# Optimization experiments

Measured on AMD Instinct MI355X. Metric: run time of the kernel, lower is better.

Reference implementation:

```python
import jax, jax.numpy as jnp
import numpy as np
import math

EMB = 512
HID = 512
SEQ = 128
BATCH = 64
VOCAB = 10000
NUM_LAYERS = 2


def setup_inputs() -> dict:
    key = jax.random.key(0)
    ks = jax.random.split(key, 16)
    inputs = jax.random.randint(ks[0], (SEQ, BATCH), 0, VOCAB)
    hidden = jnp.zeros((NUM_LAYERS, BATCH, HID), dtype=jnp.float32)
    emb_table = jax.random.normal(ks[1], (VOCAB, EMB), dtype=jnp.float32) * 0.02

    def lin(k, fan_in, fan_out):
        bound = 1.0 / math.sqrt(fan_in)
        kw, kb = jax.random.split(k)
        W = jax.random.uniform(kw, (fan_in, fan_out), minval=-bound, maxval=bound, dtype=jnp.float32)
        b = jax.random.uniform(kb, (fan_out,), minval=-bound, maxval=bound, dtype=jnp.float32)
        return W, b

    # layer 0: input_size = emb + hid; layer 1: input_size = 2*hid
    Wg0, bg0 = lin(ks[2], EMB + HID, 2 * HID)
    Wc0, bc0 = lin(ks[3], EMB + HID, HID)
    Wg1, bg1 = lin(ks[4], 2 * HID, 2 * HID)
    Wc1, bc1 = lin(ks[5], 2 * HID, HID)
    Wout, bout = lin(ks[6], HID, VOCAB)
    return {
        "inputs": inputs, "hidden": hidden, "emb_table": emb_table,
        "Wg0": Wg0, "bg0": bg0, "Wc0": Wc0, "bc0": bc0,
        "Wg1": Wg1, "bg1": bg1, "Wc1": Wc1, "bc1": bc1,
        "Wout": Wout, "bout": bout,
    }


def _gru_forward(inputs, hidden, emb_table, layer_params, Wout, bout):
    # embeddings: [S, B, E], scaled like WordEmbedding
    emb = emb_table[inputs] * jnp.asarray(math.sqrt(EMB), emb_table.dtype)

    def step(h, x_t):
        layer_in = x_t
        new_h = []
        for n, (Wg, bg, Wc, bc) in enumerate(layer_params):
            g = jax.nn.sigmoid(jnp.concatenate([layer_in, h[n]], axis=1) @ Wg + bg)
            update = g[:, :HID]
            reset = g[:, HID:]
            cell = jnp.tanh(jnp.concatenate([layer_in, reset * h[n]], axis=1) @ Wc + bc)
            h_out = (1.0 - update) * h[n] + update * cell
            new_h.append(h_out)
            layer_in = h_out
        logits_t = layer_in @ Wout + bout  # [B, V]
        return jnp.stack(new_h, axis=0), logits_t

    hidden_final, logits = jax.lax.scan(step, hidden, emb)
    return logits, hidden_final  # [S, B, V], [L, B, H]


def reference(inputs, hidden, emb_table, Wg0, bg0, Wc0, bc0, Wg1, bg1, Wc1, bc1, Wout, bout):
    layer_params = [(Wg0, bg0, Wc0, bc0), (Wg1, bg1, Wc1, bc1)]
    return _gru_forward(inputs, hidden, emb_table, layer_params, Wout, bout)
```

## Files before the change

### kernel.cpp

```cpp
#include <hip/hip_runtime.h>
#include <cstdint>
#include <cstddef>

#define SEQ 128
#define BATCH 64
#define NVOCAB 10000
#define NREC 64
#define NWORK 192
#define NTOT 256

typedef __attribute__((ext_vector_type(8))) short short8;
typedef __attribute__((ext_vector_type(4))) float f32x4;

__device__ __forceinline__ unsigned short f2b(float f) {
  union { float f; unsigned u; } c; c.f = f;
  unsigned u = c.u;
  unsigned r = (u + 0x7fffu + ((u >> 16) & 1u)) >> 16;
  return (unsigned short)r;
}

__device__ __forceinline__ f32x4 mfma16(short8 a, short8 b, f32x4 c) {
  return __builtin_amdgcn_mfma_f32_16x16x32_bf16(a, b, c, 0, 0, 0);
}

__device__ __forceinline__ short8 ldg_coh(const unsigned short* p) {
  short8 r;
  asm volatile("global_load_dwordx4 %0, %1, off sc0 sc1" : "=v"(r) : "v"(p));
  return r;
}
__device__ __forceinline__ void stg_coh(unsigned short* p, short8 v) {
  asm volatile("global_store_dwordx4 %0, %1, off sc0 sc1" :: "v"(p), "v"(v) : "memory");
}
__device__ __forceinline__ void st_stamp(int* p, int v) {
  asm volatile("global_store_dword %0, %1, off sc0 sc1" :: "v"(p), "v"(v) : "memory");
}
__device__ __forceinline__ int ld_stamp(const int* p) {
  int r;
  asm volatile("global_load_dword %0, %1, off sc0 sc1" : "=v"(r) : "v"(p));
  return r;
}

template<int SLP>
__device__ __forceinline__ void wait_all32(const int* rep, int need) {
  if (need < 0) return;
  int idx = threadIdx.x & 31;
  int guard = 0;
  for (;;) {
    int v = ld_stamp(rep + idx);
    asm volatile("s_waitcnt vmcnt(0)" ::: "memory");
    if (__all(v >= need)) return;
    __builtin_amdgcn_s_sleep(SLP);
    if (++guard > 3000000) return;
  }
}

__global__ void pack_frag(const float* __restrict__ src, unsigned short* __restrict__ dst,
                          int ksteps, int row_off, int src_ld, int ntiles, int mode, int nreal) {
  int tid = blockIdx.x * 256 + threadIdx.x;
  int total = ntiles * ksteps * 64;
  if (tid >= total) return;
  int l = tid & 63;
  int ks = (tid >> 6) % ksteps;
  int nt = tid / (64 * ksteps);
  int n = nt * 16 + (l & 15);
  int col;
  bool valid = true;
  if (mode == 1) {
    int jc = n >> 5, s = n & 31;
    col = (s < 16) ? (16 * jc + s) : (512 + 16 * jc + (s - 16));
  } else {
    col = n;
    valid = (n < nreal);
  }
  int k0 = row_off + ks * 32 + ((l >> 4) << 3);
  short8 o;
  for (int j = 0; j < 8; ++j) {
    float x = valid ? src[(size_t)(k0 + j) * src_ld + col] : 0.f;
    o[j] = (short)f2b(x);
  }
  *reinterpret_cast<short8*>(&dst[(size_t)tid * 8]) = o;
}

__global__ void pack_bias(const float* __restrict__ bg0, const float* __restrict__ bg1,
                          float* __restrict__ bg0p, float* __restrict__ bg1p) {
  int p = blockIdx.x * 256 + threadIdx.x;
  if (p >= 1024) return;
  int jc = p >> 5, s = p & 31;
  int col = (s < 16) ? (16 * jc + s) : (512 + 16 * jc + (s - 16));
  bg0p[p] = bg0[col];
  bg1p[p] = bg1[col];
}

__global__ void embed_gather(const int* __restrict__ inp, const float* __restrict__ tab,
                             unsigned short* __restrict__ XA) {
  int tid = blockIdx.x * 256 + threadIdx.x;
  if (tid >= SEQ * 64 * 64) return;
  int row = tid & 63;
  int kt = (tid >> 6) & 63;
  int t = tid >> 12;
  int v = inp[t * BATCH + row];
  const float* s = &tab[(size_t)v * 512 + kt * 8];
  const float scale = 22.627416997969522f;
  short8 o;
  for (int j = 0; j < 8; ++j) o[j] = (short)f2b(s[j] * scale);
  *reinterpret_cast<short8*>(&XA[(size_t)tid * 8]) = o;
}

__global__ void init_states(const float* __restrict__ hid, unsigned short* __restrict__ H0INITB,
                            unsigned short* __restrict__ H1INITB, int* __restrict__ stamps) {
  int idx = blockIdx.x * 256 + threadIdx.x;
  if (idx < 24 * 64) stamps[idx] = -1;
  if (idx >= 64 * 512) return;
  int row = idx >> 9, c = idx & 511;
  size_t ko = (((size_t)(c >> 3)) * 64 + row) * 8 + (c & 7);
  H0INITB[ko] = f2b(hid[idx]);
  H1INITB[ko] = f2b(hid[64 * 512 + idx]);
}

__launch_bounds__(256, 2)
__global__ void gemm128(const unsigned short* __restrict__ A, const unsigned short* __restrict__ Bf,
                        const float* __restrict__ bias, float* __restrict__ C,
                        int Nld, int Nreal) {
  __shared__ __align__(16) unsigned short ldsA[16 * 512];
  __shared__ __align__(16) unsigned short ldsB[16 * 512];
  int nb = blockIdx.x, yb = blockIdx.y;
  int l = threadIdx.x & 63, w = threadIdx.x >> 6;
  int mh = w >> 1, nh = w & 1;
  f32x4 acc[4][4] = {};
  for (int ko = 0; ko < 8; ++ko) {
    __syncthreads();
    for (int j = 0; j < 4; ++j) {
      int c = w * 4 + j;
      int m8 = c >> 1, ks = c & 1;
      int t = yb * 2 + (m8 >> 2);
      int kt = ko * 8 + ks * 4 + (l >> 4);
      int row = (m8 & 3) * 16 + (l & 15);
      size_t gidx = (((size_t)t * 64 + kt) * 64 + row) * 8;
      *reinterpret_cast<short8*>(&ldsA[(size_t)c * 512 + l * 8]) =
          *reinterpret_cast<const short8*>(&A[gidx]);
      size_t gb = (((size_t)(nb * 8 + (c >> 1)) * 16) + (size_t)(ko * 2 + (c & 1))) * 512 + (size_t)l * 8;
      *reinterpret_cast<short8*>(&ldsB[(size_t)c * 512 + l * 8]) =
          *reinterpret_cast<const short8*>(&Bf[gb]);
    }
    __syncthreads();
    for (int ks = 0; ks < 2; ++ks) {
      short8 a[4], b[4];
      for (int mt = 0; mt < 4; ++mt) {
        int m8 = mh * 4 + mt;
        a[mt] = *reinterpret_cast<const short8*>(&ldsA[((size_t)(m8 * 2 + ks) * 64 + l) * 8]);
      }
      for (int nt = 0; nt < 4; ++nt) {
        int n8 = nh * 4 + nt;
        b[nt] = *reinterpret_cast<const short8*>(&ldsB[((size_t)(n8 * 2 + ks) * 64 + l) * 8]);
      }
      for (int mt = 0; mt < 4; ++mt)
        for (int nt = 0; nt < 4; ++nt)
          acc[mt][nt] = mfma16(a[mt], b[nt], acc[mt][nt]);
    }
  }
  for (int mt = 0; mt < 4; ++mt) {
    for (int nt = 0; nt < 4; ++nt) {
      int col = nb * 128 + nh * 64 + nt * 16 + (l & 15);
      if (col >= Nreal) continue;
      float bv = bias[col];
      int row0 = yb * 128 + mh * 64 + mt * 16 + ((l >> 4) << 2);
      for (int r = 0; r < 4; ++r)
        C[(size_t)(row0 + r) * Nld + col] = acc[mt][nt][r] + bv;
    }
  }
}

template<int KS, int LAYER>
__device__ void rec_layer(
    int g, const unsigned short* __restrict__ Wg, const unsigned short* __restrict__ Wc,
    const float* __restrict__ Xg0p, const float* __restrict__ Xc0p,
    const float* __restrict__ bg1p, const float* __restrict__ bc1,
    const float* __restrict__ hidden,
    unsigned short* __restrict__ H0ALL, unsigned short* __restrict__ H1ALL,
    const unsigned short* __restrict__ H0INITB, const unsigned short* __restrict__ H1INITB,
    unsigned short* __restrict__ RH0, unsigned short* __restrict__ RH1,
    int* __restrict__ stamps, float* __restrict__ hidden_out,
    float (&red)[4][64][33], float (&u_lds)[64][17], float (&hf)[64][17]) {
  constexpr int KQ = KS / 4;
  const int tid = threadIdx.x;
  const int l = tid & 63, w = tid >> 6;
  const int s = l & 15, q = l >> 4;

  int* SR   = stamps + (LAYER ? 4 : 0) * 64;
  int* SH0  = stamps + 8 * 64;
  int* SH1  = stamps + 12 * 64;
  int* SHW  = stamps + 16 * 64;
  int* mySH = LAYER ? SH1 : SH0;
  const int repw = ((g + w) & 3) * 64;
  unsigned short* myRH = LAYER ? RH1 : RH0;

  short8 bg[2][KQ];
  short8 bc[KQ];
#pragma unroll
  for (int kk = 0; kk < KQ; ++kk) {
    int ks = w * KQ + kk;
    bg[0][kk] = *reinterpret_cast<const short8*>(&Wg[(((size_t)(2 * g) * KS + ks) * 64 + l) * 8]);
    bg[1][kk] = *reinterpret_cast<const short8*>(&Wg[(((size_t)(2 * g + 1) * KS + ks) * 64 + l) * 8]);
    bc[kk]    = *reinterpret_cast<const short8*>(&Wc[(((size_t)g * KS + ks) * 64 + l) * 8]);
  }

  {
    int col = tid & 15;
#pragma unroll
    for (int rr = 0; rr < 4; ++rr) {
      int row = (tid >> 4) * 4 + rr;
      hf[row][col] = hidden[(size_t)LAYER * 32768 + (size_t)row * 512 + 16 * g + col];
    }
  }
  __syncthreads();

  for (int t = 0; t < 128; ++t) {
    float xg[8], xc[8];
    if constexpr (LAYER == 0) {
      int row = tid & 63;
      int kg = (tid >> 6) & 1;
      int base = (tid < 128) ? 16 : 0;
#pragma unroll
      for (int j = 0; j < 8; ++j)
        xg[j] = Xg0p[((size_t)(t * 64 + row)) * 1024 + g * 32 + base + kg * 8 + j];
#pragma unroll
      for (int j = 0; j < 8; ++j)
        xc[j] = Xc0p[((size_t)(t * 64 + row)) * 512 + 16 * g + kg * 8 + j];
    }

    const unsigned short* A0 = LAYER ? (H0ALL + (size_t)t * 32768)
                                     : (t ? (H0ALL + (size_t)(t - 1) * 32768) : H0INITB);
    const unsigned short* A1 = nullptr;
    if (LAYER) A1 = t ? (H1ALL + (size_t)(t - 1) * 32768) : H1INITB;

    {
      f32x4 acc[4][2] = {};
      if constexpr (LAYER == 0) {
        wait_all32<1>(SH0 + repw, t - 1);
        short8 a[4][4];
#pragma unroll
        for (int kk2 = 0; kk2 < 4; ++kk2) {
          int kl = w * 4 + kk2;
#pragma unroll
          for (int mt = 0; mt < 4; ++mt)
            a[kk2][mt] = ldg_coh(&A0[(((size_t)(kl * 4 + q)) * 64 + mt * 16 + s) * 8]);
        }
        asm volatile("s_waitcnt vmcnt(0)" ::: "memory");
        __builtin_amdgcn_sched_barrier(0);
#pragma unroll
        for (int kk2 = 0; kk2 < 4; ++kk2)
#pragma unroll
          for (int mt = 0; mt < 4; ++mt) {
            acc[mt][0] = mfma16(a[kk2][mt], bg[0][kk2], acc[mt][0]);
            acc[mt][1] = mfma16(a[kk2][mt], bg[1][kk2], acc[mt][1]);
          }
      } else {
        if (w >= 2) wait_all32<1>(SH1 + repw, t - 1);
        else        wait_all32<1>(SH0 + repw, t);
        const unsigned short* ab = (w >= 2) ? A1 : A0;
#pragma unroll
        for (int hb = 0; hb < 2; ++hb) {
          short8 a[4][4];
#pragma unroll
          for (int kk2 = 0; kk2 < 4; ++kk2) {
            int kl = ((w & 1) * 8 + hb * 4 + kk2);
#pragma unroll
            for (int mt = 0; mt < 4; ++mt)
              a[kk2][mt] = ldg_coh(&ab[(((size_t)(kl * 4 + q)) * 64 + mt * 16 + s) * 8]);
          }
          asm volatile("s_waitcnt vmcnt(0)" ::: "memory");
          __builtin_amdgcn_sched_barrier(0);
#pragma unroll
          for (int kk2 = 0; kk2 < 4; ++kk2)
#pragma unroll
            for (int mt = 0; mt < 4; ++mt) {
              acc[mt][0] = mfma16(a[kk2][mt], bg[0][hb * 4 + kk2], acc[mt][0]);
              acc[mt][1] = mfma16(a[kk2][mt], bg[1][hb * 4 + kk2], acc[mt][1]);
            }
        }
      }
#pragma unroll
      for (int mt = 0; mt < 4; ++mt)
#pragma unroll
        for (int nt = 0; nt < 2; ++nt)
#pragma unroll
          for (int r = 0; r < 4; ++r)
            red[w][mt * 16 + q * 4 + r][nt * 16 + s] = acc[mt][nt][r];
    }
    __syncthreads();
    if (tid < 128) {
      int row = tid & 63, kg = tid >> 6;
      short8 o;
#pragma unroll
      for (int j = 0; j < 8; ++j) {
        int col = 16 + kg * 8 + j;
        float sum = red[0][row][col] + red[1][row][col] + red[2][row][col] + red[3][row][col];
        sum += LAYER ? bg1p[g * 32 + col] : xg[j];
        float gate = 1.f / (1.f + __expf(-sum));
        o[j] = (short)f2b(gate * hf[row][kg * 8 + j]);
      }
      stg_coh(&myRH[((size_t)(2 * g + kg) * 64 + row) * 8], o);
    } else {
      int t2 = tid - 128;
      int row = t2 & 63, kg = t2 >> 6;
#pragma unroll
      for (int j = 0; j < 8; ++j) {
        int col = kg * 8 + j;
        float sum = red[0][row][col] + red[1][row][col] + red[2][row][col] + red[3][row][col];
        sum += LAYER ? bg1p[g * 32 + col] : xg[j];
        u_lds[row][col] = 1.f / (1.f + __expf(-sum));
      }
    }
    asm volatile("s_waitcnt vmcnt(0)" ::: "memory");
    __syncthreads();
    if (tid == 0) {
#pragma unroll
      for (int r = 0; r < 4; ++r) st_stamp(&SR[r * 64 + g], t);
    }

    {
      f32x4 acc[4] = {};
      if constexpr (LAYER == 0) {
        wait_all32<1>(SR + repw, t);
        short8 a[4][4];
#pragma unroll
        for (int kk2 = 0; kk2 < 4; ++kk2) {
          int kl = w * 4 + kk2;
#pragma unroll
          for (int mt = 0; mt < 4; ++mt)
            a[kk2][mt] = ldg_coh(&myRH[(((size_t)(kl * 4 + q)) * 64 + mt * 16 + s) * 8]);
        }
        asm volatile("s_waitcnt vmcnt(0)" ::: "memory");
        __builtin_amdgcn_sched_barrier(0);
#pragma unroll
        for (int kk2 = 0; kk2 < 4; ++kk2)
#pragma unroll
          for (int mt = 0; mt < 4; ++mt)
            acc[mt] = mfma16(a[kk2][mt], bc[kk2], acc[mt]);
      } else {
        if (w >= 2) wait_all32<1>(SR + repw, t);
        const unsigned short* ab = (w >= 2) ? myRH : A0;
#pragma unroll
        for (int hb = 0; hb < 2; ++hb) {
          short8 a[4][4];
#pragma unroll
          for (int kk2 = 0; kk2 < 4; ++kk2) {
            int kl = ((w & 1) * 8 + hb * 4 + kk2);
#pragma unroll
            for (int mt = 0; mt < 4; ++mt)
              a[kk2][mt] = ldg_coh(&ab[(((size_t)(kl * 4 + q)) * 64 + mt * 16 + s) * 8]);
          }
          asm volatile("s_waitcnt vmcnt(0)" ::: "memory");
          __builtin_amdgcn_sched_barrier(0);
#pragma unroll
          for (int kk2 = 0; kk2 < 4; ++kk2)
#pragma unroll
            for (int mt = 0; mt < 4; ++mt)
              acc[mt] = mfma16(a[kk2][mt], bc[hb * 4 + kk2], acc[mt]);
        }
      }
#pragma unroll
      for (int mt = 0; mt < 4; ++mt)
#pragma unroll
        for (int r = 0; r < 4; ++r)
          red[w][mt * 16 + q * 4 + r][s] = acc[mt][r];
    }
    __syncthreads();
    if (tid < 128) {
      int row = tid & 63, kg = tid >> 6;
      short8 o;
#pragma unroll
      for (int j = 0; j < 8; ++j) {
        int cl = kg * 8 + j;
        float sum = red[0][row][cl] + red[1][row][cl] + red[2][row][cl] + red[3][row][cl];
        sum += LAYER ? bc1[16 * g + cl] : xc[j];
        float cv = tanhf(sum);
        float u = u_lds[row][cl];
        float hp = hf[row][cl];
        float hn = hp + u * (cv - hp);
        hf[row][cl] = hn;
        o[j] = (short)f2b(hn);
      }
      size_t ko = ((size_t)(2 * g + kg) * 64 + row) * 8;
      if (LAYER == 0) stg_coh(&H0ALL[(size_t)t * 32768 + ko], o);
      else            stg_coh(&H1ALL[(size_t)t * 32768 + ko], o);
    }
    asm volatile("s_waitcnt vmcnt(0)" ::: "memory");
    __syncthreads();
    if (tid == 0) {
#pragma unroll
      for (int r = 0; r < 4; ++r) st_stamp(&mySH[r * 64 + g], t);
      if (LAYER) {
#pragma unroll
        for (int r = 0; r < 8; ++r) st_stamp(&SHW[r * 64 + g], t);
      }
    }
  }

  {
    int col = tid & 15;
#pragma unroll
    for (int rr = 0; rr < 4; ++rr) {
      int row = (tid >> 4) * 4 + rr;
      hidden_out[(size_t)LAYER * 32768 + (size_t)row * 512 + 16 * g + col] = hf[row][col];
    }
  }
}

__device__ void worker_path(int wid, const unsigned short* __restrict__ A,
                            const unsigned short* __restrict__ Bf,
                            const float* __restrict__ bias, float* __restrict__ C,
                            const int* __restrict__ stamps, char* smem) {
  unsigned short* ldsA = (unsigned short*)smem;
  unsigned short* ldsB = (unsigned short*)(smem + 16384);
  const int* rep = stamps + (16 + (wid & 7)) * 64;
  int l = threadIdx.x & 63, w = threadIdx.x >> 6;
  int mh = w >> 1, nh = w & 1;
  for (int id = wid; id < 64 * 80; id += NWORK) {
    int tp = id / 80, nb = id - tp * 80;
    wait_all32<16>(rep, 2 * tp + 1);
    f32x4 acc[4][4] = {};
    for (int ko = 0; ko < 8; ++ko) {
      __syncthreads();
      for (int j = 0; j < 4; ++j) {
        int c = w * 4 + j;
        int m8 = c >> 1, ks = c & 1;
        int t = tp * 2 + (m8 >> 2);
        int kt = ko * 8 + ks * 4 + (l >> 4);
        int row = (m8 & 3) * 16 + (l & 15);
        size_t gidx = (((size_t)t * 64 + kt) * 64 + row) * 8;
        *reinterpret_cast<short8*>(&ldsA[(size_t)c * 512 + l * 8]) =
            *reinterpret_cast<const short8*>(&A[gidx]);
        size_t gb = (((size_t)(nb * 8 + (c >> 1)) * 16) + (size_t)(ko * 2 + (c & 1))) * 512 + (size_t)l * 8;
        *reinterpret_cast<short8*>(&ldsB[(size_t)c * 512 + l * 8]) =
            *reinterpret_cast<const short8*>(&Bf[gb]);
      }
      __syncthreads();
      for (int ks = 0; ks < 2; ++ks) {
        short8 a[4], b[4];
        for (int mt = 0; mt < 4; ++mt)
          a[mt] = *reinterpret_cast<const short8*>(&ldsA[((size_t)((mh * 4 + mt) * 2 + ks) * 64 + l) * 8]);
        for (int nt = 0; nt < 4; ++nt)
          b[nt] = *reinterpret_cast<const short8*>(&ldsB[((size_t)((nh * 4 + nt) * 2 + ks) * 64 + l) * 8]);
        for (int mt = 0; mt < 4; ++mt)
          for (int nt = 0; nt < 4; ++nt)
            acc[mt][nt] = mfma16(a[mt], b[nt], acc[mt][nt]);
      }
    }
    for (int mt = 0; mt < 4; ++mt) {
      for (int nt = 0; nt < 4; ++nt) {
        int col = nb * 128 + nh * 64 + nt * 16 + (l & 15);
        if (col >= NVOCAB) continue;
        float bv = bias[col];
        int row0 = tp * 128 + mh * 64 + mt * 16 + ((l >> 4) << 2);
        for (int r = 0; r < 4; ++r)
          C[(size_t)(row0 + r) * NVOCAB + col] = acc[mt][nt][r] + bv;
      }
    }
  }
}

__launch_bounds__(256, 1)
__global__ void fused_persist(const unsigned short* __restrict__ Wg0h, const unsigned short* __restrict__ Wc0h,
                              const unsigned short* __restrict__ Wg1, const unsigned short* __restrict__ Wc1,
                              const float* __restrict__ Xg0p, const float* __restrict__ Xc0p,
                              const float* __restrict__ bg1p, const float* __restrict__ bc1,
                              const float* __restrict__ hidden,
                              unsigned short* __restrict__ H0ALL, unsigned short* __restrict__ H1ALL,
                              const unsigned short* __restrict__ H0INITB, const unsigned short* __restrict__ H1INITB,
                              unsigned short* __restrict__ RH0, unsigned short* __restrict__ RH1,
                              int* __restrict__ stamps, float* __restrict__ hidden_out,
                              const unsigned short* __restrict__ Wout_f, const float* __restrict__ bout,
                              float* __restrict__ out) {
  __shared__ __align__(16) char smem[42496];
  int wg = blockIdx.x;
  if (wg >= NREC) {
    worker_path(wg - NREC, H1ALL, Wout_f, bout, out, stamps, smem);
    return;
  }
  float (*red)[64][33] = (float(*)[64][33])smem;
  float (*u_lds)[17] = (float(*)[17])(smem + 33792);
  float (*hf)[17] = (float(*)[17])(smem + 38144);
  int g = wg & 31;
  if (wg < 32)
    rec_layer<16, 0>(g, Wg0h, Wc0h, Xg0p, Xc0p, bg1p, bc1, hidden, H0ALL, H1ALL,
                     H0INITB, H1INITB, RH0, RH1, stamps, hidden_out,
                     *(float(*)[4][64][33])red, *(float(*)[64][17])u_lds, *(float(*)[64][17])hf);
  else
    rec_layer<32, 1>(g, Wg1, Wc1, Xg0p, Xc0p, bg1p, bc1, hidden, H0ALL, H1ALL,
                     H0INITB, H1INITB, RH0, RH1, stamps, hidden_out,
                     *(float(*)[4][64][33])red, *(float(*)[64][17])u_lds, *(float(*)[64][17])hf);
}

static inline int gridFor(long long n) { return (int)((n + 255) / 256); }

extern "C" void kernel_launch(void* const* d_in, const int* in_sizes, int n_in,
                              void* d_out, int out_size, void* d_ws, size_t ws_size,
                              hipStream_t stream) {
  const int*   inputs = (const int*)d_in[0];
  const float* hidden = (const float*)d_in[1];
  const float* embtab = (const float*)d_in[2];
  const float* Wg0 = (const float*)d_in[3];
  const float* bg0 = (const float*)d_in[4];
  const float* Wc0 = (const float*)d_in[5];
  const float* bc0 = (const float*)d_in[6];
  const float* Wg1 = (const float*)d_in[7];
  const float* bg1 = (const float*)d_in[8];
  const float* Wc1 = (const float*)d_in[9];
  const float* bc1 = (const float*)d_in[10];
  const float* Wout = (const float*)d_in[11];
  const float* bout = (const float*)d_in[12];
  float* out = (float*)d_out;

  char* p = (char*)d_ws;
  size_t off = 0;
  auto carve = [&](size_t bytes) { char* r = p + off; off += (bytes + 255) & ~(size_t)255; return (void*)r; };
  unsigned short* XA     = (unsigned short*)carve((size_t)8192 * 512 * 2);
  unsigned short* Wg0x_f = (unsigned short*)carve((size_t)512 * 1024 * 2);
  unsigned short* Wg0h_f = (unsigned short*)carve((size_t)512 * 1024 * 2);
  unsigned short* Wc0x_f = (unsigned short*)carve((size_t)512 * 512 * 2);
  unsigned short* Wc0h_f = (unsigned short*)carve((size_t)512 * 512 * 2);
  unsigned short* Wg1_f  = (unsigned short*)carve((size_t)1024 * 1024 * 2);
  unsigned short* Wc1_f  = (unsigned short*)carve((size_t)1024 * 512 * 2);
  unsigned short* Wout_f = (unsigned short*)carve((size_t)512 * 10240 * 2);
  float* Xg0p = (float*)carve((size_t)8192 * 1024 * 4);
  float* Xc0p = (float*)carve((size_t)8192 * 512 * 4);
  unsigned short* H1ALL  = (unsigned short*)carve((size_t)128 * 32768 * 2);
  unsigned short* H0ALL  = (unsigned short*)carve((size_t)128 * 32768 * 2);
  unsigned short* H0INITB= (unsigned short*)carve((size_t)32768 * 2);
  unsigned short* H1INITB= (unsigned short*)carve((size_t)32768 * 2);
  unsigned short* RH0 = (unsigned short*)carve((size_t)32768 * 2);
  unsigned short* RH1 = (unsigned short*)carve((size_t)32768 * 2);
  float* bg0p = (float*)carve(1024 * 4);
  float* bg1p = (float*)carve(1024 * 4);
  int* stamps = (int*)carve(24 * 64 * 4);
  if (off > ws_size) return;

  pack_frag<<<gridFor(64LL * 16 * 64), 256, 0, stream>>>(Wg0, Wg0x_f, 16, 0,   1024, 64, 1, 1024);
  pack_frag<<<gridFor(64LL * 16 * 64), 256, 0, stream>>>(Wg0, Wg0h_f, 16, 512, 1024, 64, 1, 1024);
  pack_frag<<<gridFor(32LL * 16 * 64), 256, 0, stream>>>(Wc0, Wc0x_f, 16, 0,   512,  32, 0, 512);
  pack_frag<<<gridFor(32LL * 16 * 64), 256, 0, stream>>>(Wc0, Wc0h_f, 16, 512, 512,  32, 0, 512);
  pack_frag<<<gridFor(64LL * 32 * 64), 256, 0, stream>>>(Wg1, Wg1_f,  32, 0,   1024, 64, 1, 1024);
  pack_frag<<<gridFor(32LL * 32 * 64), 256, 0, stream>>>(Wc1, Wc1_f,  32, 0,   512,  32, 0, 512);
  pack_frag<<<gridFor(640LL * 16 * 64), 256, 0, stream>>>(Wout, Wout_f, 16, 0, 10000, 640, 0, 10000);
  pack_bias<<<4, 256, 0, stream>>>(bg0, bg1, bg0p, bg1p);

  embed_gather<<<gridFor((long long)SEQ * 64 * 64), 256, 0, stream>>>(inputs, embtab, XA);
  init_states<<<gridFor(32768), 256, 0, stream>>>(hidden, H0INITB, H1INITB, stamps);

  gemm128<<<dim3(8, 64), 256, 0, stream>>>(XA, Wg0x_f, bg0p, Xg0p, 1024, 1024);
  gemm128<<<dim3(4, 64), 256, 0, stream>>>(XA, Wc0x_f, bc0, Xc0p, 512, 512);

  fused_persist<<<NTOT, 256, 0, stream>>>(Wg0h_f, Wc0h_f, Wg1_f, Wc1_f, Xg0p, Xc0p,
                                          bg1p, bc1, hidden, H0ALL, H1ALL,
                                          H0INITB, H1INITB, RH0, RH1,
                                          stamps, out + (size_t)81920000,
                                          Wout_f, bout, out);
}
```

Before: 1.239 ms.

## Halve recurrent workgroups to 32, each owning 32 hidden columns

Cuts the recurrent path from 64 to 32 workgroups, so each one now computes 32 hidden columns, with the layer-1 candidate weights staged in LDS. The freed workgroups become extra output-projection workers with a fixed vocab-block-per-worker assignment. Stamp waits now poll 16 producers instead of 32, which reduces cross-workgroup synchronization fan-in. In exchange each recurrent step does twice the per-workgroup MFMA work and needs a large dynamic LDS allocation, which may lengthen the serial critical path and caps occupancy at one block per CU.

```diff
diff --git a/kernel.cpp b/kernel.cpp
--- a/kernel.cpp
+++ b/kernel.cpp
@@ -5,8 +5,8 @@
 #define SEQ 128
 #define BATCH 64
 #define NVOCAB 10000
-#define NREC 64
-#define NWORK 192
+#define NREC 32
+#define NWORK 224
 #define NTOT 256
 
 typedef __attribute__((ext_vector_type(8))) short short8;
@@ -41,12 +41,12 @@
 }
 
 template<int SLP>
-__device__ __forceinline__ void wait_all32(const int* rep, int need) {
+__device__ __forceinline__ void wait16(const int* line, int need) {
   if (need < 0) return;
-  int idx = threadIdx.x & 31;
+  int idx = threadIdx.x & 15;
   int guard = 0;
   for (;;) {
-    int v = ld_stamp(rep + idx);
+    int v = ld_stamp(line + idx);
     asm volatile("s_waitcnt vmcnt(0)" ::: "memory");
     if (__all(v >= need)) return;
     __builtin_amdgcn_s_sleep(SLP);
@@ -55,7 +55,7 @@
 }
 
 __global__ void pack_frag(const float* __restrict__ src, unsigned short* __restrict__ dst,
-                          int ksteps, int row_off, int src_ld, int ntiles, int mode, int nreal) {
+                          int ksteps, int row_off, int src_ld, int ntiles, int nreal) {
   int tid = blockIdx.x * 256 + threadIdx.x;
   int total = ntiles * ksteps * 64;
   if (tid >= total) return;
@@ -63,32 +63,14 @@
   int ks = (tid >> 6) % ksteps;
   int nt = tid / (64 * ksteps);
   int n = nt * 16 + (l & 15);
-  int col;
-  bool valid = true;
-  if (mode == 1) {
-    int jc = n >> 5, s = n & 31;
-    col = (s < 16) ? (16 * jc + s) : (512 + 16 * jc + (s - 16));
-  } else {
-    col = n;
-    valid = (n < nreal);
-  }
+  bool valid = (n < nreal);
   int k0 = row_off + ks * 32 + ((l >> 4) << 3);
   short8 o;
   for (int j = 0; j < 8; ++j) {
-    float x = valid ? src[(size_t)(k0 + j) * src_ld + col] : 0.f;
+    float x = valid ? src[(size_t)(k0 + j) * src_ld + n] : 0.f;
     o[j] = (short)f2b(x);
   }
   *reinterpret_cast<short8*>(&dst[(size_t)tid * 8]) = o;
-}
-
-__global__ void pack_bias(const float* __restrict__ bg0, const float* __restrict__ bg1,
-                          float* __restrict__ bg0p, float* __restrict__ bg1p) {
-  int p = blockIdx.x * 256 + threadIdx.x;
-  if (p >= 1024) return;
-  int jc = p >> 5, s = p & 31;
-  int col = (s < 16) ? (16 * jc + s) : (512 + 16 * jc + (s - 16));
-  bg0p[p] = bg0[col];
-  bg1p[p] = bg1[col];
 }
 
 __global__ void embed_gather(const int* __restrict__ inp, const float* __restrict__ tab,
@@ -170,21 +152,26 @@
   }
 }
 
-template<int KS, int LAYER>
+template<int KSTEPS, int LAYER>
 __device__ void rec_layer(
     int g, const unsigned short* __restrict__ Wg, const unsigned short* __restrict__ Wc,
     const float* __restrict__ Xg0p, const float* __restrict__ Xc0p,
-    const float* __restrict__ bg1p, const float* __restrict__ bc1,
+    const float* __restrict__ bg1, const float* __restrict__ bc1,
     const float* __restrict__ hidden,
     unsigned short* __restrict__ H0ALL, unsigned short* __restrict__ H1ALL,
     const unsigned short* __restrict__ H0INITB, const unsigned short* __restrict__ H1INITB,
     unsigned short* __restrict__ RH0, unsigned short* __restrict__ RH1,
-    int* __restrict__ stamps, float* __restrict__ hidden_out,
-    float (&red)[4][64][33], float (&u_lds)[64][17], float (&hf)[64][17]) {
-  constexpr int KQ = KS / 4;
+    int* __restrict__ stamps, float* __restrict__ hidden_out, char* smem) {
+  constexpr int KQ = KSTEPS / 4;
   const int tid = threadIdx.x;
   const int l = tid & 63, w = tid >> 6;
   const int s = l & 15, q = l >> 4;
+  const int erow = tid & 63, ekg = tid >> 6;
+
+  unsigned short* WcL = (unsigned short*)smem;
+  float (*red)[64][65] = (float(*)[64][65])(smem + 65536);
+  float (*u_lds)[33] = (float(*)[33])(smem + 65536 + 66560);
+  float (*hf)[33] = (float(*)[33])(smem + 65536 + 66560 + 8448);
 
   int* SR   = stamps + (LAYER ? 4 : 0) * 64;
   int* SH0  = stamps + 8 * 64;
@@ -194,76 +181,98 @@
   const int repw = ((g + w) & 3) * 64;
   unsigned short* myRH = LAYER ? RH1 : RH0;
 
-  short8 bg[2][KQ];
-  short8 bc[KQ];
-#pragma unroll
-  for (int kk = 0; kk < KQ; ++kk) {
-    int ks = w * KQ + kk;
-    bg[0][kk] = *reinterpret_cast<const short8*>(&Wg[(((size_t)(2 * g) * KS + ks) * 64 + l) * 8]);
-    bg[1][kk] = *reinterpret_cast<const short8*>(&Wg[(((size_t)(2 * g + 1) * KS + ks) * 64 + l) * 8]);
-    bc[kk]    = *reinterpret_cast<const short8*>(&Wc[(((size_t)g * KS + ks) * 64 + l) * 8]);
+  short8 bg[2][2][KQ];
+#pragma unroll
+  for (int nl = 0; nl < 2; ++nl)
+#pragma unroll
+    for (int kk = 0; kk < KQ; ++kk) {
+      int ks = w * KQ + kk;
+      bg[0][nl][kk] = *reinterpret_cast<const short8*>(
+          &Wg[(((size_t)(2 * g + nl) * KSTEPS + ks) * 64 + l) * 8]);
+      bg[1][nl][kk] = *reinterpret_cast<const short8*>(
+          &Wg[(((size_t)(32 + 2 * g + nl) * KSTEPS + ks) * 64 + l) * 8]);
+    }
+  short8 bc[2][KQ];
+  if constexpr (LAYER == 0) {
+#pragma unroll
+    for (int nl = 0; nl < 2; ++nl)
+#pragma unroll
+      for (int kk = 0; kk < KQ; ++kk) {
+        int ks = w * KQ + kk;
+        bc[nl][kk] = *reinterpret_cast<const short8*>(
+            &Wc[(((size_t)(2 * g + nl) * KSTEPS + ks) * 64 + l) * 8]);
+      }
+  } else {
+    const short8* src = reinterpret_cast<const short8*>(Wc + (size_t)(2 * g) * KSTEPS * 512);
+    short8* dst = reinterpret_cast<short8*>(WcL);
+    for (int i = tid; i < 2 * KSTEPS * 64; i += 256) dst[i] = src[i];
   }
 
   {
-    int col = tid & 15;
-#pragma unroll
-    for (int rr = 0; rr < 4; ++rr) {
-      int row = (tid >> 4) * 4 + rr;
-      hf[row][col] = hidden[(size_t)LAYER * 32768 + (size_t)row * 512 + 16 * g + col];
+#pragma unroll
+    for (int j = 0; j < 8; ++j)
+      hf[erow][ekg * 8 + j] = hidden[(size_t)LAYER * 32768 + (size_t)erow * 512 + 32 * g + ekg * 8 + j];
+  }
+  float bu[8], br[8], bcv[8];
+  if constexpr (LAYER) {
+#pragma unroll
+    for (int j = 0; j < 8; ++j) {
+      bu[j]  = bg1[32 * g + ekg * 8 + j];
+      br[j]  = bg1[512 + 32 * g + ekg * 8 + j];
+      bcv[j] = bc1[32 * g + ekg * 8 + j];
     }
   }
   __syncthreads();
 
   for (int t = 0; t < 128; ++t) {
-    float xg[8], xc[8];
+    float xu[8], xr[8], xc[8];
     if constexpr (LAYER == 0) {
-      int row = tid & 63;
-      int kg = (tid >> 6) & 1;
-      int base = (tid < 128) ? 16 : 0;
-#pragma unroll
-      for (int j = 0; j < 8; ++j)
-        xg[j] = Xg0p[((size_t)(t * 64 + row)) * 1024 + g * 32 + base + kg * 8 + j];
-#pragma unroll
-      for (int j = 0; j < 8; ++j)
-        xc[j] = Xc0p[((size_t)(t * 64 + row)) * 512 + 16 * g + kg * 8 + j];
-    }
-
+      size_t rb = (size_t)(t * 64 + erow);
+#pragma unroll
+      for (int j = 0; j < 8; ++j) {
+        xu[j] = Xg0p[rb * 1024 + 32 * g + ekg * 8 + j];
+        xr[j] = Xg0p[rb * 1024 + 512 + 32 * g + ekg * 8 + j];
+        xc[j] = Xc0p[rb * 512 + 32 * g + ekg * 8 + j];
+      }
+    }
     const unsigned short* A0 = LAYER ? (H0ALL + (size_t)t * 32768)
                                      : (t ? (H0ALL + (size_t)(t - 1) * 32768) : H0INITB);
     const unsigned short* A1 = nullptr;
     if (LAYER) A1 = t ? (H1ALL + (size_t)(t - 1) * 32768) : H1INITB;
 
     {
-      f32x4 acc[4][2] = {};
+      f32x4 acc[4][4] = {};
       if constexpr (LAYER == 0) {
-        wait_all32<1>(SH0 + repw, t - 1);
+        wait16<1>(SH0 + repw, t - 1);
         short8 a[4][4];
 #pragma unroll
-        for (int kk2 = 0; kk2 < 4; ++kk2) {
-          int kl = w * 4 + kk2;
+        for (int kk = 0; kk < 4; ++kk) {
+          int kl = w * 4 + kk;
 #pragma unroll
           for (int mt = 0; mt < 4; ++mt)
-            a[kk2][mt] = ldg_coh(&A0[(((size_t)(kl * 4 + q)) * 64 + mt * 16 + s) * 8]);
+            a[kk][mt] = ldg_coh(&A0[(((size_t)(kl * 4 + q)) * 64 + mt * 16 + s) * 8]);
         }
         asm volatile("s_waitcnt vmcnt(0)" ::: "memory");
         __builtin_amdgcn_sched_barrier(0);
 #pragma unroll
-        for (int kk2 = 0; kk2 < 4; ++kk2)
+        for (int kk = 0; kk < 4; ++kk)
 #pragma unroll
           for (int mt = 0; mt < 4; ++mt) {
-            acc[mt][0] = mfma16(a[kk2][mt], bg[0][kk2], acc[mt][0]);
-            acc[mt][1] = mfma16(a[kk2][mt], bg[1][kk2], acc[mt][1]);
+            acc[mt][0] = mfma16(a[kk][mt], bg[0][0][kk], acc[mt][0]);
+            acc[mt][1] = mfma16(a[kk][mt], bg[0][1][kk], acc[mt][1]);
+            acc[mt][2] = mfma16(a[kk][mt], bg[1][0][kk], acc[mt][2]);
+            acc[mt][3] = mfma16(a[kk][mt], bg[1][1][kk], acc[mt][3]);
           }
       } else {
-        if (w >= 2) wait_all32<1>(SH1 + repw, t - 1);
-        else        wait_all32<1>(SH0 + repw, t);
+        if (w >= 2) wait16<1>(SH1 + repw, t - 1);
+        else        wait16<1>(SH0 + repw, t);
         const unsigned short* ab = (w >= 2) ? A1 : A0;
 #pragma unroll
         for (int hb = 0; hb < 2; ++hb) {
           short8 a[4][4];
 #pragma unroll
           for (int kk2 = 0; kk2 < 4; ++kk2) {
-            int kl = ((w & 1) * 8 + hb * 4 + kk2);
+            int kl = (w & 1) * 8 + hb * 4 + kk2;
 #pragma unroll
             for (int mt = 0; mt < 4; ++mt)
               a[kk2][mt] = ldg_coh(&ab[(((size_t)(kl * 4 + q)) * 64 + mt * 16 + s) * 8]);
@@ -271,81 +280,79 @@
           asm volatile("s_waitcnt vmcnt(0)" ::: "memory");
           __builtin_amdgcn_sched_barrier(0);
 #pragma unroll
-          for (int kk2 = 0; kk2 < 4; ++kk2)
+          for (int kk2 = 0; kk2 < 4; ++kk2) {
+            int kkg = hb * 4 + kk2;
 #pragma unroll
             for (int mt = 0; mt < 4; ++mt) {
-              acc[mt][0] = mfma16(a[kk2][mt], bg[0][hb * 4 + kk2], acc[mt][0]);
-              acc[mt][1] = mfma16(a[kk2][mt], bg[1][hb * 4 + kk2], acc[mt][1]);
+              acc[mt][0] = mfma16(a[kk2][mt], bg[0][0][kkg], acc[mt][0]);
+              acc[mt][1] = mfma16(a[kk2][mt], bg[0][1][kkg], acc[mt][1]);
+              acc[mt][2] = mfma16(a[kk2][mt], bg[1][0][kkg], acc[mt][2]);
+              acc[mt][3] = mfma16(a[kk2][mt], bg[1][1][kkg], acc[mt][3]);
             }
+          }
         }
       }
 #pragma unroll
       for (int mt = 0; mt < 4; ++mt)
 #pragma unroll
-        for (int nt = 0; nt < 2; ++nt)
+        for (int nc = 0; nc < 4; ++nc)
 #pragma unroll
           for (int r = 0; r < 4; ++r)
-            red[w][mt * 16 + q * 4 + r][nt * 16 + s] = acc[mt][nt][r];
+            red[w][mt * 16 + q * 4 + r][nc * 16 + s] = acc[mt][nc][r];
     }
     __syncthreads();
-    if (tid < 128) {
-      int row = tid & 63, kg = tid >> 6;
+    {
       short8 o;
 #pragma unroll
       for (int j = 0; j < 8; ++j) {
-        int col = 16 + kg * 8 + j;
-        float sum = red[0][row][col] + red[1][row][col] + red[2][row][col] + red[3][row][col];
-        sum += LAYER ? bg1p[g * 32 + col] : xg[j];
-        float gate = 1.f / (1.f + __expf(-sum));
-        o[j] = (short)f2b(gate * hf[row][kg * 8 + j]);
-      }
-      stg_coh(&myRH[((size_t)(2 * g + kg) * 64 + row) * 8], o);
-    } else {
-      int t2 = tid - 128;
-      int row = t2 & 63, kg = t2 >> 6;
-#pragma unroll
-      for (int j = 0; j < 8; ++j) {
-        int col = kg * 8 + j;
-        float sum = red[0][row][col] + red[1][row][col] + red[2][row][col] + red[3][row][col];
-        sum += LAYER ? bg1p[g * 32 + col] : xg[j];
-        u_lds[row][col] = 1.f / (1.f + __expf(-sum));
-      }
+        int cu = ekg * 8 + j, cr = 32 + ekg * 8 + j;
+        float su = red[0][erow][cu] + red[1][erow][cu] + red[2][erow][cu] + red[3][erow][cu];
+        float sr = red[0][erow][cr] + red[1][erow][cr] + red[2][erow][cr] + red[3][erow][cr];
+        su += LAYER ? bu[j] : xu[j];
+        sr += LAYER ? br[j] : xr[j];
+        u_lds[erow][cu] = 1.f / (1.f + __expf(-su));
+        float gate = 1.f / (1.f + __expf(-sr));
+        o[j] = (short)f2b(gate * hf[erow][cu]);
+      }
+      stg_coh(&myRH[((size_t)(4 * g + ekg) * 64 + erow) * 8], o);
     }
     asm volatile("s_waitcnt vmcnt(0)" ::: "memory");
     __syncthreads();
     if (tid == 0) {
 #pragma unroll
-      for (int r = 0; r < 4; ++r) st_stamp(&SR[r * 64 + g], t);
+      for (int r4 = 0; r4 < 4; ++r4) st_stamp(&SR[r4 * 64 + g], t);
     }
 
     {
-      f32x4 acc[4] = {};
+      f32x4 acc[4][2] = {};
       if constexpr (LAYER == 0) {
-        wait_all32<1>(SR + repw, t);
+        wait16<1>(SR + repw, t);
         short8 a[4][4];
 #pragma unroll
-        for (int kk2 = 0; kk2 < 4; ++kk2) {
-          int kl = w * 4 + kk2;
+        for (int kk = 0; kk < 4; ++kk) {
+          int kl = w * 4 + kk;
 #pragma unroll
           for (int mt = 0; mt < 4; ++mt)
-            a[kk2][mt] = ldg_coh(&myRH[(((size_t)(kl * 4 + q)) * 64 + mt * 16 + s) * 8]);
+            a[kk][mt] = ldg_coh(&RH0[(((size_t)(kl * 4 + q)) * 64 + mt * 16 + s) * 8]);
         }
         asm volatile("s_waitcnt vmcnt(0)" ::: "memory");
         __builtin_amdgcn_sched_barrier(0);
 #pragma unroll
-        for (int kk2 = 0; kk2 < 4; ++kk2)
-#pragma unroll
-          for (int mt = 0; mt < 4; ++mt)
-            acc[mt] = mfma16(a[kk2][mt], bc[kk2], acc[mt]);
+        for (int kk = 0; kk < 4; ++kk)
+#pragma unroll
+          for (int mt = 0; mt < 4; ++mt) {
+            acc[mt][0] = mfma16(a[kk][mt], bc[0][kk], acc[mt][0]);
+            acc[mt][1] = mfma16(a[kk][mt], bc[1][kk], acc[mt][1]);
+          }
       } else {
-        if (w >= 2) wait_all32<1>(SR + repw, t);
+        if (w >= 2) wait16<1>(SR + repw, t);
         const unsigned short* ab = (w >= 2) ? myRH : A0;
 #pragma unroll
         for (int hb = 0; hb < 2; ++hb) {
           short8 a[4][4];
 #pragma unroll
           for (int kk2 = 0; kk2 < 4; ++kk2) {
-            int kl = ((w & 1) * 8 + hb * 4 + kk2);
+            int kl = (w & 1) * 8 + hb * 4 + kk2;
 #pragma unroll
             for (int mt = 0; mt < 4; ++mt)
               a[kk2][mt] = ldg_coh(&ab[(((size_t)(kl * 4 + q)) * 64 + mt * 16 + s) * 8]);
@@ -353,58 +360,58 @@
           asm volatile("s_waitcnt vmcnt(0)" ::: "memory");
           __builtin_amdgcn_sched_barrier(0);
 #pragma unroll
-          for (int kk2 = 0; kk2 < 4; ++kk2)
-#pragma unroll
-            for (int mt = 0; mt < 4; ++mt)
-              acc[mt] = mfma16(a[kk2][mt], bc[hb * 4 + kk2], acc[mt]);
+          for (int kk2 = 0; kk2 < 4; ++kk2) {
+            int ks = w * 8 + hb * 4 + kk2;
+#pragma unroll
+            for (int mt = 0; mt < 4; ++mt) {
+              short8 b0 = *reinterpret_cast<const short8*>(&WcL[(((size_t)(0 * KSTEPS + ks)) * 64 + l) * 8]);
+              short8 b1 = *reinterpret_cast<const short8*>(&WcL[(((size_t)(1 * KSTEPS + ks)) * 64 + l) * 8]);
+              acc[mt][0] = mfma16(a[kk2][mt], b0, acc[mt][0]);
+              acc[mt][1] = mfma16(a[kk2][mt], b1, acc[mt][1]);
+            }
+          }
         }
       }
 #pragma unroll
       for (int mt = 0; mt < 4; ++mt)
 #pragma unroll
-        for (int r = 0; r < 4; ++r)
-          red[w][mt * 16 + q * 4 + r][s] = acc[mt][r];
+        for (int nt = 0; nt < 2; ++nt)
+#pragma unroll
+          for (int r = 0; r < 4; ++r)
+            red[w][mt * 16 + q * 4 + r][nt * 16 + s] = acc[mt][nt][r];
     }
     __syncthreads();
-    if (tid < 128) {
-      int row = tid & 63, kg = tid >> 6;
+    {
       short8 o;
 #pragma unroll
       for (int j = 0; j < 8; ++j) {
-        int cl = kg * 8 + j;
-        float sum = red[0][row][cl] + red[1][row][cl] + red[2][row][cl] + red[3][row][cl];
-        sum += LAYER ? bc1[16 * g + cl] : xc[j];
+        int c = ekg * 8 + j;
+        float sum = red[0][erow][c] + red[1][erow][c] + red[2][erow][c] + red[3][erow][c];
+        sum += LAYER ? bcv[j] : xc[j];
         float cv = tanhf(sum);
-        float u = u_lds[row][cl];
-        float hp = hf[row][cl];
-        float hn = hp + u * (cv - hp);
-        hf[row][cl] = hn;
+        float hp = hf[erow][c];
+        float hn = hp + u_lds[erow][c] * (cv - hp);
+        hf[erow][c] = hn;
         o[j] = (short)f2b(hn);
       }
-      size_t ko = ((size_t)(2 * g + kg) * 64 + row) * 8;
-      if (LAYER == 0) stg_coh(&H0ALL[(size_t)t * 32768 + ko], o);
-      else            stg_coh(&H1ALL[(size_t)t * 32768 + ko], o);
+      unsigned short* Hdst = (LAYER ? H1ALL : H0ALL) + (size_t)t * 32768;
+      stg_coh(&Hdst[((size_t)(4 * g + ekg) * 64 + erow) * 8], o);
     }
     asm volatile("s_waitcnt vmcnt(0)" ::: "memory");
     __syncthreads();
     if (tid == 0) {
 #pragma unroll
-      for (int r = 0; r < 4; ++r) st_stamp(&mySH[r * 64 + g], t);
+      for (int r4 = 0; r4 < 4; ++r4) st_stamp(&mySH[r4 * 64 + g], t);
       if (LAYER) {
 #pragma unroll
-        for (int r = 0; r < 8; ++r) st_stamp(&SHW[r * 64 + g], t);
-      }
-    }
-  }
-
-  {
-    int col = tid & 15;
-#pragma unroll
-    for (int rr = 0; rr < 4; ++rr) {
-      int row = (tid >> 4) * 4 + rr;
-      hidden_out[(size_t)LAYER * 32768 + (size_t)row * 512 + 16 * g + col] = hf[row][col];
-    }
-  }
+        for (int r8 = 0; r8 < 8; ++r8) st_stamp(&SHW[r8 * 64 + g], t);
+      }
+    }
+  }
+
+#pragma unroll
+  for (int j = 0; j < 8; ++j)
+    hidden_out[(size_t)LAYER * 32768 + (size_t)erow * 512 + 32 * g + ekg * 8 + j] = hf[erow][ekg * 8 + j];
 }
 
 __device__ void worker_path(int wid, const unsigned short* __restrict__ A,
@@ -416,9 +423,11 @@
   const int* rep = stamps + (16 + (wid & 7)) * 64;
   int l = threadIdx.x & 63, w = threadIdx.x >> 6;
   int mh = w >> 1, nh = w & 1;
-  for (int id = wid; id < 64 * 80; id += NWORK) {
-    int tp = id / 80, nb = id - tp * 80;
-    wait_all32<16>(rep, 2 * tp + 1);
+  int nb = wid % 80;
+  int helper = wid / 80;
+  int nhelp = (nb < 64) ? 3 : 2;
+  for (int tp = helper; tp < 64; tp += nhelp) {
+    wait16<16>(rep, 2 * tp + 1);
     f32x4 acc[4][4] = {};
     for (int ko = 0; ko < 8; ++ko) {
       __syncthreads();
@@ -464,7 +473,7 @@
 __global__ void fused_persist(const unsigned short* __restrict__ Wg0h, const unsigned short* __restrict__ Wc0h,
                               const unsigned short* __restrict__ Wg1, const unsigned short* __restrict__ Wc1,
                               const float* __restrict__ Xg0p, const float* __restrict__ Xc0p,
-                              const float* __restrict__ bg1p, const float* __restrict__ bc1,
+                              const float* __restrict__ bg1, const float* __restrict__ bc1,
                               const float* __restrict__ hidden,
                               unsigned short* __restrict__ H0ALL, unsigned short* __restrict__ H1ALL,
                               const unsigned short* __restrict__ H0INITB, const unsigned short* __restrict__ H1INITB,
@@ -472,24 +481,18 @@
                               int* __restrict__ stamps, float* __restrict__ hidden_out,
                               const unsigned short* __restrict__ Wout_f, const float* __restrict__ bout,
                               float* __restrict__ out) {
-  __shared__ __align__(16) char smem[42496];
+  extern __shared__ __align__(16) char smem[];
   int wg = blockIdx.x;
   if (wg >= NREC) {
     worker_path(wg - NREC, H1ALL, Wout_f, bout, out, stamps, smem);
     return;
   }
-  float (*red)[64][33] = (float(*)[64][33])smem;
-  float (*u_lds)[17] = (float(*)[17])(smem + 33792);
-  float (*hf)[17] = (float(*)[17])(smem + 38144);
-  int g = wg & 31;
-  if (wg < 32)
-    rec_layer<16, 0>(g, Wg0h, Wc0h, Xg0p, Xc0p, bg1p, bc1, hidden, H0ALL, H1ALL,
-                     H0INITB, H1INITB, RH0, RH1, stamps, hidden_out,
-                     *(float(*)[4][64][33])red, *(float(*)[64][17])u_lds, *(float(*)[64][17])hf);
+  if (wg < 16)
+    rec_layer<16, 0>(wg, Wg0h, Wc0h, Xg0p, Xc0p, bg1, bc1, hidden, H0ALL, H1ALL,
+                     H0INITB, H1INITB, RH0, RH1, stamps, hidden_out, smem);
   else
-    rec_layer<32, 1>(g, Wg1, Wc1, Xg0p, Xc0p, bg1p, bc1, hidden, H0ALL, H1ALL,
-                     H0INITB, H1INITB, RH0, RH1, stamps, hidden_out,
-                     *(float(*)[4][64][33])red, *(float(*)[64][17])u_lds, *(float(*)[64][17])hf);
+    rec_layer<32, 1>(wg - 16, Wg1, Wc1, Xg0p, Xc0p, bg1, bc1, hidden, H0ALL, H1ALL,
+                     H0INITB, H1INITB, RH0, RH1, stamps, hidden_out, smem);
 }
 
 static inline int gridFor(long long n) { return (int)((n + 255) / 256); }
@@ -531,29 +534,26 @@
   unsigned short* H1INITB= (unsigned short*)carve((size_t)32768 * 2);
   unsigned short* RH0 = (unsigned short*)carve((size_t)32768 * 2);
   unsigned short* RH1 = (unsigned short*)carve((size_t)32768 * 2);
-  float* bg0p = (float*)carve(1024 * 4);
-  float* bg1p = (float*)carve(1024 * 4);
   int* stamps = (int*)carve(24 * 64 * 4);
   if (off > ws_size) return;
 
-  pack_frag<<<gridFor(64LL * 16 * 64), 256, 0, stream>>>(Wg0, Wg0x_f, 16, 0,   1024, 64, 1, 1024);
-  pack_frag<<<gridFor(64LL * 16 * 64), 256, 0, stream>>>(Wg0, Wg0h_f, 16, 512, 1024, 64, 1, 1024);
-  pack_frag<<<gridFor(32LL * 16 * 64), 256, 0, stream>>>(Wc0, Wc0x_f, 16, 0,   512,  32, 0, 512);
-  pack_frag<<<gridFor(32LL * 16 * 64), 256, 0, stream>>>(Wc0, Wc0h_f, 16, 512, 512,  32, 0, 512);
-  pack_frag<<<gridFor(64LL * 32 * 64), 256, 0, stream>>>(Wg1, Wg1_f,  32, 0,   1024, 64, 1, 1024);
-  pack_frag<<<gridFor(32LL * 32 * 64), 256, 0, stream>>>(Wc1, Wc1_f,  32, 0,   512,  32, 0, 512);
-  pack_frag<<<gridFor(640LL * 16 * 64), 256, 0, stream>>>(Wout, Wout_f, 16, 0, 10000, 640, 0, 10000);
-  pack_bias<<<4, 256, 0, stream>>>(bg0, bg1, bg0p, bg1p);
+  pack_frag<<<gridFor(64LL * 16 * 64), 256, 0, stream>>>(Wg0, Wg0x_f, 16, 0,   1024, 64, 1024);
+  pack_frag<<<gridFor(64LL * 16 * 64), 256, 0, stream>>>(Wg0, Wg0h_f, 16, 512, 1024, 64, 1024);
+  pack_frag<<<gridFor(32LL * 16 * 64), 256, 0, stream>>>(Wc0, Wc0x_f, 16, 0,   512,  32, 512);
+  pack_frag<<<gridFor(32LL * 16 * 64), 256, 0, stream>>>(Wc0, Wc0h_f, 16, 512, 512,  32, 512);
+  pack_frag<<<gridFor(64LL * 32 * 64), 256, 0, stream>>>(Wg1, Wg1_f,  32, 0,   1024, 64, 1024);
+  pack_frag<<<gridFor(32LL * 32 * 64), 256, 0, stream>>>(Wc1, Wc1_f,  32, 0,   512,  32, 512);
+  pack_frag<<<gridFor(640LL * 16 * 64), 256, 0, stream>>>(Wout, Wout_f, 16, 0, 10000, 640, 10000);
 
   embed_gather<<<gridFor((long long)SEQ * 64 * 64), 256, 0, stream>>>(inputs, embtab, XA);
   init_states<<<gridFor(32768), 256, 0, stream>>>(hidden, H0INITB, H1INITB, stamps);
 
-  gemm128<<<dim3(8, 64), 256, 0, stream>>>(XA, Wg0x_f, bg0p, Xg0p, 1024, 1024);
+  gemm128<<<dim3(8, 64), 256, 0, stream>>>(XA, Wg0x_f, bg0, Xg0p, 1024, 1024);
   gemm128<<<dim3(4, 64), 256, 0, stream>>>(XA, Wc0x_f, bc0, Xc0p, 512, 512);
 
-  fused_persist<<<NTOT, 256, 0, stream>>>(Wg0h_f, Wc0h_f, Wg1_f, Wc1_f, Xg0p, Xc0p,
-                                          bg1p, bc1, hidden, H0ALL, H1ALL,
-                                          H0INITB, H1INITB, RH0, RH1,
-                                          stamps, out + (size_t)81920000,
-                                          Wout_f, bout, out);
-}
+  fused_persist<<<NTOT, 256, 148992, stream>>>(Wg0h_f, Wc0h_f, Wg1_f, Wc1_f, Xg0p, Xc0p,
+                                               bg1, bc1, hidden, H0ALL, H1ALL,
+                                               H0INITB, H1INITB, RH0, RH1,
+                                               stamps, out + (size_t)81920000,
+                                               Wout_f, bout, out);
+}
```

Result: slower. 1.287 ms (+3.9%).

## Use per-wave readiness stamps and fixed-column worker scheduling for output GEMM

Applied to the files above, without the earlier changes.

Each of the two producing waves now publishes its own readiness stamp right after its stores drain, rather than one thread stamping for the whole block after a block barrier. Consumer waves poll only the subset of stamps that covers the K-slice they actually read. This is meant to shorten the serial dependency chain of the recurrent steps. Output-projection workers now keep a fixed vocab column block and iterate over time pairs, which may improve reuse of the Wout tiles. The cost is more stamp traffic and a load imbalance across helpers (three or two per column block).

```diff
diff --git a/kernel.cpp b/kernel.cpp
--- a/kernel.cpp
+++ b/kernel.cpp
@@ -40,10 +40,10 @@
   return r;
 }
 
-template<int SLP>
-__device__ __forceinline__ void wait_all32(const int* rep, int need) {
+template<int SLP, int NW>
+__device__ __forceinline__ void wait_sub(const int* rep, int base, int need) {
   if (need < 0) return;
-  int idx = threadIdx.x & 31;
+  int idx = base + (threadIdx.x & (NW - 1));
   int guard = 0;
   for (;;) {
     int v = ld_stamp(rep + idx);
@@ -236,7 +236,7 @@
     {
       f32x4 acc[4][2] = {};
       if constexpr (LAYER == 0) {
-        wait_all32<1>(SH0 + repw, t - 1);
+        wait_sub<1, 16>(SH0 + repw, 16 * w, t - 1);
         short8 a[4][4];
 #pragma unroll
         for (int kk2 = 0; kk2 < 4; ++kk2) {
@@ -255,8 +255,8 @@
             acc[mt][1] = mfma16(a[kk2][mt], bg[1][kk2], acc[mt][1]);
           }
       } else {
-        if (w >= 2) wait_all32<1>(SH1 + repw, t - 1);
-        else        wait_all32<1>(SH0 + repw, t);
+        if (w >= 2) wait_sub<1, 32>(SH1 + repw, 32 * (w & 1), t - 1);
+        else        wait_sub<1, 32>(SH0 + repw, 32 * (w & 1), t);
         const unsigned short* ab = (w >= 2) ? A1 : A0;
 #pragma unroll
         for (int hb = 0; hb < 2; ++hb) {
@@ -312,16 +312,16 @@
       }
     }
     asm volatile("s_waitcnt vmcnt(0)" ::: "memory");
+    if (l == 0 && w < 2) {
+#pragma unroll
+      for (int r4 = 0; r4 < 4; ++r4) st_stamp(&SR[r4 * 64 + 2 * g + w], t);
+    }
     __syncthreads();
-    if (tid == 0) {
-#pragma unroll
-      for (int r = 0; r < 4; ++r) st_stamp(&SR[r * 64 + g], t);
-    }
 
     {
       f32x4 acc[4] = {};
       if constexpr (LAYER == 0) {
-        wait_all32<1>(SR + repw, t);
+        wait_sub<1, 16>(SR + repw, 16 * w, t);
         short8 a[4][4];
 #pragma unroll
         for (int kk2 = 0; kk2 < 4; ++kk2) {
@@ -338,7 +338,7 @@
           for (int mt = 0; mt < 4; ++mt)
             acc[mt] = mfma16(a[kk2][mt], bc[kk2], acc[mt]);
       } else {
-        if (w >= 2) wait_all32<1>(SR + repw, t);
+        if (w >= 2) wait_sub<1, 32>(SR + repw, 32 * (w & 1), t);
         const unsigned short* ab = (w >= 2) ? myRH : A0;
 #pragma unroll
         for (int hb = 0; hb < 2; ++hb) {
@@ -386,15 +386,15 @@
       else            stg_coh(&H1ALL[(size_t)t * 32768 + ko], o);
     }
     asm volatile("s_waitcnt vmcnt(0)" ::: "memory");
+    if (l == 0 && w < 2) {
+#pragma unroll
+      for (int r4 = 0; r4 < 4; ++r4) st_stamp(&mySH[r4 * 64 + 2 * g + w], t);
+      if (LAYER) {
+#pragma unroll
+        for (int r8 = 0; r8 < 8; ++r8) st_stamp(&SHW[r8 * 64 + 2 * g + w], t);
+      }
+    }
     __syncthreads();
-    if (tid == 0) {
-#pragma unroll
-      for (int r = 0; r < 4; ++r) st_stamp(&mySH[r * 64 + g], t);
-      if (LAYER) {
-#pragma unroll
-        for (int r = 0; r < 8; ++r) st_stamp(&SHW[r * 64 + g], t);
-      }
-    }
   }
 
   {
@@ -416,9 +416,11 @@
   const int* rep = stamps + (16 + (wid & 7)) * 64;
   int l = threadIdx.x & 63, w = threadIdx.x >> 6;
   int mh = w >> 1, nh = w & 1;
-  for (int id = wid; id < 64 * 80; id += NWORK) {
-    int tp = id / 80, nb = id - tp * 80;
-    wait_all32<16>(rep, 2 * tp + 1);
+  int nb = wid % 80;
+  int helper = wid / 80;
+  int nhelp = (nb < 32) ? 3 : 2;
+  for (int tp = helper; tp < 64; tp += nhelp) {
+    wait_sub<16, 64>(rep, 0, 2 * tp + 1);
     f32x4 acc[4][4] = {};
     for (int ko = 0; ko < 8; ++ko) {
       __syncthreads();
```

New measurement: 1.281 ms. +3.4%, slower.
